# Kernel optimization log

Measured on AMD Instinct MI355X. Metric: run time of the kernel, lower is better.

The kernel has to match this reference:

```python
import jax, jax.numpy as jnp
import numpy as np

D_MODEL = 256
N_HEAD = 8
D_FF = 2048
BATCH = 4
TOK_PER_BATCH = 4096
N = BATCH * TOK_PER_BATCH  # 16384 total queries == total keys
L = 32  # neighbors per query
EPS = 1e-5


def _layer_norm(x, g, b):
    mu = jnp.mean(x, axis=-1, keepdims=True)
    var = jnp.mean(jnp.square(x - mu), axis=-1, keepdims=True)
    return (x - mu) * jax.lax.rsqrt(var + EPS) * g + b


def setup_inputs() -> dict:
    key = jax.random.key(0)
    ks = jax.random.split(key, 16)
    d, f = D_MODEL, D_FF
    s = 1.0 / np.sqrt(d)
    inp = {
        "src": jax.random.normal(ks[0], (N, d), dtype=jnp.float32),
        "index_pair": jax.random.randint(ks[1], (N, L), 0, TOK_PER_BATCH, dtype=jnp.int64),
        "query_batch_cnt": jnp.full((BATCH,), TOK_PER_BATCH, dtype=jnp.int32),
        "key_batch_cnt": jnp.full((BATCH,), TOK_PER_BATCH, dtype=jnp.int32),
        "index_pair_batch": jnp.repeat(jnp.arange(BATCH, dtype=jnp.int32), TOK_PER_BATCH),
        "Wq": jax.random.normal(ks[2], (d, d), dtype=jnp.float32) * s,
        "bq": jnp.zeros((d,), jnp.float32),
        "Wk": jax.random.normal(ks[3], (d, d), dtype=jnp.float32) * s,
        "bk": jnp.zeros((d,), jnp.float32),
        "Wv": jax.random.normal(ks[4], (d, d), dtype=jnp.float32) * s,
        "bv": jnp.zeros((d,), jnp.float32),
        "Wo": jax.random.normal(ks[5], (d, d), dtype=jnp.float32) * s,
        "bo": jnp.zeros((d,), jnp.float32),
        "W1": jax.random.normal(ks[6], (d, f), dtype=jnp.float32) * s,
        "b1": jnp.zeros((f,), jnp.float32),
        "W2": jax.random.normal(ks[7], (f, d), dtype=jnp.float32) * (1.0 / np.sqrt(f)),
        "b2": jnp.zeros((d,), jnp.float32),
        "g1": jnp.ones((d,), jnp.float32),
        "be1": jnp.zeros((d,), jnp.float32),
        "g2": jnp.ones((d,), jnp.float32),
        "be2": jnp.zeros((d,), jnp.float32),
    }
    return inp


def _attention(src, index_pair, key_batch_cnt, index_pair_batch,
               Wq, bq, Wk, bk, Wv, bv, Wo, bo):
    n, d = src.shape
    hd = d // N_HEAD
    scale = hd ** -0.5
    q = (src @ Wq + bq).reshape(n, N_HEAD, hd) * scale
    k = src @ Wk + bk
    v = src @ Wv + bv
    # exclusive cumsum -> start offset of each batch's key segment
    key_start = jnp.cumsum(key_batch_cnt) - key_batch_cnt          # [B]
    offs = key_start[index_pair_batch]                             # [N]
    valid = index_pair >= 0                                        # [N, L]
    idx = jnp.where(valid, index_pair + offs[:, None].astype(index_pair.dtype), 0)
    kg = k[idx].reshape(n, L, N_HEAD, hd)                          # gathered keys
    vg = v[idx].reshape(n, L, N_HEAD, hd)                          # gathered values
    logits = jnp.einsum("nhd,nlhd->nhl", q, kg)
    logits = jnp.where(valid[:, None, :], logits, jnp.float32(-1e9))
    attn = jax.nn.softmax(logits, axis=-1)
    out = jnp.einsum("nhl,nlhd->nhd", attn, vg).reshape(n, d)
    return out @ Wo + bo


def reference(src, index_pair, query_batch_cnt, key_batch_cnt, index_pair_batch,
              Wq, bq, Wk, bk, Wv, bv, Wo, bo, W1, b1, W2, b2, g1, be1, g2, be2):
    src2 = _attention(src, index_pair, key_batch_cnt, index_pair_batch,
                      Wq, bq, Wk, bk, Wv, bv, Wo, bo)
    x = _layer_norm(src + src2, g1, be1)
    ff = jax.nn.relu(x @ W1 + b1) @ W2 + b2
    return _layer_norm(x + ff, g2, be2)
```

## Files before the change

kernel.cpp:

```cpp
#include <hip/hip_runtime.h>
#include <hip/hip_bf16.h>
#include <cstddef>
#include <cstdint>

#define D_MODEL 256
#define N_TOK   16384
#define NHEAD   8
#define HDIM    32
#define LNEIGH  32
#define DFF     2048

#define SMEM_LN32 (8192 + 65536)

typedef short bf16x8 __attribute__((ext_vector_type(8)));
typedef float f32x4  __attribute__((ext_vector_type(4)));

__device__ __forceinline__ float b2f(short s) {
    unsigned u = ((unsigned)(unsigned short)s) << 16;
    return __builtin_bit_cast(float, u);
}

__device__ __forceinline__ void gload_lds16(const void* g, void* l) {
    auto* gp = reinterpret_cast<const __attribute__((address_space(1))) uint32_t*>(
        reinterpret_cast<uintptr_t>(g));
    auto* lp = reinterpret_cast<__attribute__((address_space(3))) uint32_t*>(
        reinterpret_cast<uintptr_t>(l));
    __builtin_amdgcn_global_load_lds(gp, lp, 16, 0, 0);
}

__global__ __launch_bounds__(256) void gemm_bt(
    const __hip_bfloat16* __restrict__ A, int lda,
    const __hip_bfloat16* __restrict__ Bt, int ldb,
    const float* __restrict__ bias,
    __hip_bfloat16* __restrict__ outb, int ldc,
    int M, int N, int K, int relu)
{
    __shared__ short Asm[2][128 * 32];
    __shared__ short Bsm[2][128 * 32];

    const int tid  = threadIdx.x;
    const int lane = tid & 63;
    const int wid  = tid >> 6;
    const int wr   = wid >> 1;
    const int wc   = wid & 1;
    const int bm   = blockIdx.y * 128;
    const int bn   = blockIdx.x * 128;

    f32x4 acc[4][4] = {};
    const int srow = lane >> 2;
    const int seg  = (lane & 3) * 8;

    auto stage = [&](int buf, int k0) {
        #pragma unroll
        for (int t = 0; t < 2; ++t) {
            int rbase = wid * 32 + t * 16;
            gload_lds16(A  + (size_t)(bm + rbase + srow) * lda + k0 + seg, &Asm[buf][rbase * 32]);
            gload_lds16(Bt + (size_t)(bn + rbase + srow) * ldb + k0 + seg, &Bsm[buf][rbase * 32]);
        }
    };

    const int nk = K >> 5;
    stage(0, 0);
    __syncthreads();

    for (int kk = 0; kk < nk; ++kk) {
        const int cur = kk & 1;
        if (kk + 1 < nk) stage(cur ^ 1, (kk + 1) << 5);

        bf16x8 a[4], b[4];
        #pragma unroll
        for (int i = 0; i < 4; ++i)
            a[i] = *(const bf16x8*)&Asm[cur][(wr * 64 + i * 16 + (lane & 15)) * 32 + (lane >> 4) * 8];
        #pragma unroll
        for (int j = 0; j < 4; ++j)
            b[j] = *(const bf16x8*)&Bsm[cur][(wc * 64 + j * 16 + (lane & 15)) * 32 + (lane >> 4) * 8];
        #pragma unroll
        for (int i = 0; i < 4; ++i)
            #pragma unroll
            for (int j = 0; j < 4; ++j)
                acc[i][j] = __builtin_amdgcn_mfma_f32_16x16x32_bf16(a[i], b[j], acc[i][j], 0, 0, 0);
        __syncthreads();
    }

    #pragma unroll
    for (int i = 0; i < 4; ++i) {
        int rbase = bm + wr * 64 + i * 16 + ((lane >> 4) << 2);
        #pragma unroll
        for (int j = 0; j < 4; ++j) {
            int col = bn + wc * 64 + j * 16 + (lane & 15);
            float bval = bias ? bias[col] : 0.0f;
            #pragma unroll
            for (int r = 0; r < 4; ++r) {
                int row = rbase + r;
                float v = acc[i][j][r] + bval;
                if (relu) v = fmaxf(v, 0.0f);
                outb[(size_t)row * ldc + col] = __float2bfloat16(v);
            }
        }
    }
}

__global__ __launch_bounds__(512) void gemm_bk64_ln32(
    const __hip_bfloat16* __restrict__ A, int lda,
    const __hip_bfloat16* __restrict__ Bt, int ldb,
    const float* __restrict__ bias,
    const float* __restrict__ residf,
    const __hip_bfloat16* __restrict__ residb,
    const float* __restrict__ g,
    const float* __restrict__ be,
    float* __restrict__ outf,
    __hip_bfloat16* __restrict__ outb,
    int K)
{
    extern __shared__ char smem[];
    short* AsmB = (short*)smem;
    short* BsmB = (short*)(smem + 8192);
    float* lnS  = (float*)smem;
    float* lnS2 = (float*)(smem + 1024);
    float* rmu  = (float*)(smem + 2048);
    float* rrs  = (float*)(smem + 2176);

    const int tid  = threadIdx.x;
    const int lane = tid & 63;
    const int wid  = tid >> 6;
    const int wr   = wid >> 2;
    const int wc   = wid & 3;
    const int bm   = blockIdx.x * 32;
    const int lo   = lane & 15;
    const int hi   = lane >> 4;

    f32x4 acc[4] = {};

    const int srow8 = lane >> 3;
    const int sc    = lane & 7;
    const int ssw   = ((sc ^ srow8) << 3);

    auto stage = [&](int buf, int k0) {
        if (wid < 4)
            gload_lds16(A + (size_t)(bm + wid * 8 + srow8) * lda + k0 + ssw,
                        AsmB + buf * 2048 + (wid * 8) * 64);
        #pragma unroll
        for (int t = 0; t < 4; ++t) {
            int rb = wid * 32 + t * 8;
            gload_lds16(Bt + (size_t)(rb + srow8) * ldb + k0 + ssw,
                        BsmB + buf * 16384 + rb * 64);
        }
    };

    const int nk = K >> 6;
    stage(0, 0);
    __syncthreads();

    for (int kk = 0; kk < nk; ++kk) {
        const int cur = kk & 1;
        if (kk + 1 < nk) stage(cur ^ 1, (kk + 1) << 6);

        const short* Ab = AsmB + cur * 2048;
        const short* Bb = BsmB + cur * 16384;
        #pragma unroll
        for (int ks = 0; ks < 2; ++ks) {
            const int csw = ((ks * 4 + hi) ^ (lo & 7)) << 3;
            bf16x8 a = *(const bf16x8*)&Ab[(wr * 16 + lo) * 64 + csw];
            bf16x8 b[4];
            #pragma unroll
            for (int j = 0; j < 4; ++j)
                b[j] = *(const bf16x8*)&Bb[(wc * 64 + j * 16 + lo) * 64 + csw];
            #pragma unroll
            for (int j = 0; j < 4; ++j)
                acc[j] = __builtin_amdgcn_mfma_f32_16x16x32_bf16(a, b[j], acc[j], 0, 0, 0);
        }
        __syncthreads();
    }

    float ps[4] = {}, ps2[4] = {};
    #pragma unroll
    for (int j = 0; j < 4; ++j) {
        int col = wc * 64 + j * 16 + lo;
        float bval = bias ? bias[col] : 0.0f;
        #pragma unroll
        for (int r = 0; r < 4; ++r) {
            int row = bm + wr * 16 + hi * 4 + r;
            float v = acc[j][r] + bval;
            size_t o = (size_t)row * 256 + col;
            if (residf) v += residf[o];
            if (residb) v += __bfloat162float(residb[o]);
            acc[j][r] = v;
            ps[r]  += v;
            ps2[r] += v * v;
        }
    }
    #pragma unroll
    for (int r = 0; r < 4; ++r) {
        #pragma unroll
        for (int m = 1; m < 16; m <<= 1) {
            ps[r]  += __shfl_xor(ps[r],  m);
            ps2[r] += __shfl_xor(ps2[r], m);
        }
    }
    if (lo == 0) {
        #pragma unroll
        for (int r = 0; r < 4; ++r) {
            int rl = wr * 16 + hi * 4 + r;
            lnS[wid * 32 + rl]  = ps[r];
            lnS2[wid * 32 + rl] = ps2[r];
        }
    }
    __syncthreads();
    if (tid < 32) {
        int base = (tid >> 4) * 4;
        float s  = lnS[base * 32 + tid] + lnS[(base + 1) * 32 + tid]
                 + lnS[(base + 2) * 32 + tid] + lnS[(base + 3) * 32 + tid];
        float s2 = lnS2[base * 32 + tid] + lnS2[(base + 1) * 32 + tid]
                 + lnS2[(base + 2) * 32 + tid] + lnS2[(base + 3) * 32 + tid];
        float mu  = s * (1.0f / 256.0f);
        float var = s2 * (1.0f / 256.0f) - mu * mu;
        rmu[tid] = mu;
        rrs[tid] = rsqrtf(var + 1e-5f);
    }
    __syncthreads();

    #pragma unroll
    for (int j = 0; j < 4; ++j) {
        int col = wc * 64 + j * 16 + lo;
        float gg = g[col], bb = be[col];
        #pragma unroll
        for (int r = 0; r < 4; ++r) {
            int rl = wr * 16 + hi * 4 + r;
            float v = (acc[j][r] - rmu[rl]) * rrs[rl] * gg + bb;
            size_t o = (size_t)(bm + rl) * 256 + col;
            if (outf) outf[o] = v;
            if (outb) outb[o] = __float2bfloat16(v);
        }
    }
}

__global__ __launch_bounds__(256) void gemm_qkv(
    const __hip_bfloat16* __restrict__ A,
    const __hip_bfloat16* __restrict__ Bt,
    const float* __restrict__ bias,
    float* __restrict__ qf,
    __hip_bfloat16* __restrict__ kvb)
{
    __shared__ short Asm[2][128 * 32];
    __shared__ short Bsm[2][128 * 32];

    const int tid  = threadIdx.x;
    const int lane = tid & 63;
    const int wid  = tid >> 6;
    const int wr   = wid >> 1;
    const int wc   = wid & 1;
    const int bm   = blockIdx.y * 128;
    const int bn   = blockIdx.x * 128;

    f32x4 acc[4][4] = {};
    const int srow = lane >> 2;
    const int seg  = (lane & 3) * 8;

    auto stage = [&](int buf, int k0) {
        #pragma unroll
        for (int t = 0; t < 2; ++t) {
            int rbase = wid * 32 + t * 16;
            gload_lds16(A  + (size_t)(bm + rbase + srow) * 256 + k0 + seg, &Asm[buf][rbase * 32]);
            gload_lds16(Bt + (size_t)(bn + rbase + srow) * 256 + k0 + seg, &Bsm[buf][rbase * 32]);
        }
    };

    stage(0, 0);
    __syncthreads();
    for (int kk = 0; kk < 8; ++kk) {
        const int cur = kk & 1;
        if (kk + 1 < 8) stage(cur ^ 1, (kk + 1) << 5);
        bf16x8 a[4], b[4];
        #pragma unroll
        for (int i = 0; i < 4; ++i)
            a[i] = *(const bf16x8*)&Asm[cur][(wr * 64 + i * 16 + (lane & 15)) * 32 + (lane >> 4) * 8];
        #pragma unroll
        for (int j = 0; j < 4; ++j)
            b[j] = *(const bf16x8*)&Bsm[cur][(wc * 64 + j * 16 + (lane & 15)) * 32 + (lane >> 4) * 8];
        #pragma unroll
        for (int i = 0; i < 4; ++i)
            #pragma unroll
            for (int j = 0; j < 4; ++j)
                acc[i][j] = __builtin_amdgcn_mfma_f32_16x16x32_bf16(a[i], b[j], acc[i][j], 0, 0, 0);
        __syncthreads();
    }

    const bool isq = (bn < 256);
    #pragma unroll
    for (int i = 0; i < 4; ++i) {
        int rbase = bm + wr * 64 + i * 16 + ((lane >> 4) << 2);
        #pragma unroll
        for (int j = 0; j < 4; ++j) {
            int col = bn + wc * 64 + j * 16 + (lane & 15);
            float bval = bias[col];
            #pragma unroll
            for (int r = 0; r < 4; ++r) {
                int row = rbase + r;
                float v = acc[i][j][r] + bval;
                if (isq) qf[(size_t)row * 256 + col] = v;
                else     kvb[(size_t)row * 512 + (col - 256)] = __float2bfloat16(v);
            }
        }
    }
}

__global__ __launch_bounds__(256) void cvt_f2b(
    const float* __restrict__ x, __hip_bfloat16* __restrict__ y, int n)
{
    int i = (blockIdx.x * 256 + threadIdx.x) * 4;
    if (i >= n) return;
    float4 v = *(const float4*)(x + i);
    y[i + 0] = __float2bfloat16(v.x);
    y[i + 1] = __float2bfloat16(v.y);
    y[i + 2] = __float2bfloat16(v.z);
    y[i + 3] = __float2bfloat16(v.w);
}

__global__ __launch_bounds__(256) void cvt_wt_tiled(
    const float* __restrict__ W, __hip_bfloat16* __restrict__ Wt,
    int K, int N, int ldo, float scale)
{
    __shared__ float t[32][33];
    const int n0 = blockIdx.x * 32;
    const int k0 = blockIdx.y * 32;
    const int tx = threadIdx.x & 31;
    const int ty = threadIdx.x >> 5;
    #pragma unroll
    for (int i = 0; i < 32; i += 8)
        t[ty + i][tx] = W[(size_t)(k0 + ty + i) * N + n0 + tx];
    __syncthreads();
    #pragma unroll
    for (int i = 0; i < 32; i += 8)
        Wt[(size_t)(n0 + ty + i) * ldo + k0 + tx] = __float2bfloat16(t[tx][ty + i] * scale);
}

__global__ __launch_bounds__(256) void cvt_w3_tiled(
    const float* __restrict__ Wa, const float* __restrict__ Wb,
    const float* __restrict__ Wc, __hip_bfloat16* __restrict__ Wt,
    float scale_a)
{
    __shared__ float t[32][33];
    const int n0 = blockIdx.x * 32;
    const int k0 = blockIdx.y * 32;
    const float* W = (n0 < 256) ? Wa : (n0 < 512 ? Wb : Wc);
    const float sc = (n0 < 256) ? scale_a : 1.0f;
    const int ncol = n0 & 255;
    const int tx = threadIdx.x & 31;
    const int ty = threadIdx.x >> 5;
    #pragma unroll
    for (int i = 0; i < 32; i += 8)
        t[ty + i][tx] = W[(size_t)(k0 + ty + i) * 256 + ncol + tx];
    __syncthreads();
    #pragma unroll
    for (int i = 0; i < 32; i += 8)
        Wt[(size_t)(n0 + ty + i) * 256 + k0 + tx] = __float2bfloat16(t[tx][ty + i] * sc);
}

__global__ __launch_bounds__(768) void make_bqkv(
    const float* __restrict__ bq, const float* __restrict__ bk,
    const float* __restrict__ bv, const int* __restrict__ kbc, int nb,
    float* __restrict__ o, int* __restrict__ ks, float qs)
{
    int i = threadIdx.x;
    if (i < 256)      o[i] = bq[i] * qs;
    else if (i < 512) o[i] = bk[i - 256];
    else              o[i] = bv[i - 512];
    if (i < nb) {
        int acc = 0;
        for (int j = 0; j < i; ++j) acc += kbc[j];
        ks[i] = acc;
    }
}

__global__ __launch_bounds__(256) void attn_wave(
    const float* __restrict__ qf,
    const __hip_bfloat16* __restrict__ kvb,
    const int* __restrict__ index_pair,
    const int* __restrict__ ipb,
    const int* __restrict__ key_start,
    __hip_bfloat16* __restrict__ out)
{
    const int w    = threadIdx.x >> 6;
    const int lane = threadIdx.x & 63;
    const int bid  = blockIdx.x;
    const int n  = (bid & 7) * 2048 + (bid >> 3) * 4 + w;
    const int c  = lane & 31;
    const int pp = lane >> 5;

    int raw = index_pair[(size_t)n * LNEIGH + c];
    int ks  = key_start[ipb[n]];
    int gi0 = (raw >= 0) ? raw + ks : -1;

    const float* qp = qf + (size_t)n * 256 + c * 8;
    float4 q0 = *(const float4*)(qp);
    float4 q1 = *(const float4*)(qp + 4);

    int gi[16];
    #pragma unroll
    for (int i = 0; i < 16; ++i) gi[i] = __shfl(gi0, 2 * i + pp);

    bf16x8 kr[16];
    #pragma unroll
    for (int i = 0; i < 16; ++i) {
        int g = gi[i] < 0 ? 0 : gi[i];
        kr[i] = *(const bf16x8*)(kvb + (size_t)g * 512 + c * 8);
    }

    float s[16];
    #pragma unroll
    for (int i = 0; i < 16; ++i) {
        float t = q0.x * b2f(kr[i][0]) + q0.y * b2f(kr[i][1])
                + q0.z * b2f(kr[i][2]) + q0.w * b2f(kr[i][3])
                + q1.x * b2f(kr[i][4]) + q1.y * b2f(kr[i][5])
                + q1.z * b2f(kr[i][6]) + q1.w * b2f(kr[i][7]);
        t += __shfl_xor(t, 1);
        t += __shfl_xor(t, 2);
        s[i] = (gi[i] < 0) ? -1e9f : t;
    }

    bf16x8 vr[16];
    #pragma unroll
    for (int i = 0; i < 16; ++i) {
        int g = gi[i] < 0 ? 0 : gi[i];
        vr[i] = *(const bf16x8*)(kvb + (size_t)g * 512 + 256 + c * 8);
    }

    float m = s[0];
    #pragma unroll
    for (int i = 1; i < 16; ++i) m = fmaxf(m, s[i]);
    m = fmaxf(m, __shfl_xor(m, 32));
    float tot = 0.0f;
    #pragma unroll
    for (int i = 0; i < 16; ++i) { s[i] = __expf(s[i] - m); tot += s[i]; }
    tot += __shfl_xor(tot, 32);
    const float inv = 1.0f / tot;

    float a[8] = {};
    #pragma unroll
    for (int i = 0; i < 16; ++i) {
        float wt = s[i] * inv;
        #pragma unroll
        for (int j = 0; j < 8; ++j) a[j] += wt * b2f(vr[i][j]);
    }
    #pragma unroll
    for (int j = 0; j < 8; ++j) a[j] += __shfl_xor(a[j], 32);

    if (pp == 0) {
        bf16x8 ov;
        #pragma unroll
        for (int j = 0; j < 8; ++j)
            ov[j] = __builtin_bit_cast(short, __float2bfloat16(a[j]));
        *(bf16x8*)((short*)out + (size_t)n * 256 + c * 8) = ov;
    }
}

extern "C" void kernel_launch(void* const* d_in, const int* in_sizes, int n_in,
                              void* d_out, int out_size, void* d_ws, size_t ws_size,
                              hipStream_t stream)
{
    const float* src = (const float*)d_in[0];
    const int*   index_pair = (const int*)d_in[1];
    const int*   kbc = (const int*)d_in[3];
    const int*   ipb = (const int*)d_in[4];
    const float* Wq = (const float*)d_in[5];
    const float* bq = (const float*)d_in[6];
    const float* Wk = (const float*)d_in[7];
    const float* bk = (const float*)d_in[8];
    const float* Wv = (const float*)d_in[9];
    const float* bv = (const float*)d_in[10];
    const float* Wo = (const float*)d_in[11];
    const float* bo = (const float*)d_in[12];
    const float* W1 = (const float*)d_in[13];
    const float* b1 = (const float*)d_in[14];
    const float* W2 = (const float*)d_in[15];
    const float* b2 = (const float*)d_in[16];
    const float* g1 = (const float*)d_in[17];
    const float* be1 = (const float*)d_in[18];
    const float* g2 = (const float*)d_in[19];
    const float* be2 = (const float*)d_in[20];
    float* out = (float*)d_out;
    const int nb = in_sizes[3];

    char* ws = (char*)d_ws;
    const size_t O_SRCBF = 0;
    const size_t O_QF    = 8388608;
    const size_t O_KVB   = 25165824;
    const size_t O_ATTN  = 41943040;
    const size_t O_HC    = 0;
    const size_t O_XBF   = 67108864;
    const size_t O_WQKV  = 75497472;
    const size_t O_WO    = O_WQKV + 768 * 256 * 2;
    const size_t O_W1    = O_WO + 256 * 256 * 2;
    const size_t O_W2    = O_W1 + (size_t)DFF * 256 * 2;
    const size_t O_BQKV  = O_W2 + (size_t)DFF * 256 * 2;
    const size_t O_KS    = O_BQKV + 768 * 4;

    __hip_bfloat16* src_bf  = (__hip_bfloat16*)(ws + O_SRCBF);
    float*          qf      = (float*)(ws + O_QF);
    __hip_bfloat16* kvb     = (__hip_bfloat16*)(ws + O_KVB);
    __hip_bfloat16* attn_bf = (__hip_bfloat16*)(ws + O_ATTN);
    __hip_bfloat16* hc      = (__hip_bfloat16*)(ws + O_HC);
    __hip_bfloat16* x_bf    = (__hip_bfloat16*)(ws + O_XBF);
    __hip_bfloat16* WqkvT   = (__hip_bfloat16*)(ws + O_WQKV);
    __hip_bfloat16* WoT     = (__hip_bfloat16*)(ws + O_WO);
    __hip_bfloat16* W1T     = (__hip_bfloat16*)(ws + O_W1);
    __hip_bfloat16* W2T     = (__hip_bfloat16*)(ws + O_W2);
    float*          bqkv    = (float*)(ws + O_BQKV);
    int*            ksbuf   = (int*)(ws + O_KS);

    const dim3 blk(256);
    const float qscale = 0.17677669529663687f;

    hipFuncSetAttribute(reinterpret_cast<const void*>(gemm_bk64_ln32),
                        hipFuncAttributeMaxDynamicSharedMemorySize, SMEM_LN32);

    cvt_f2b<<<N_TOK * D_MODEL / 4 / 256, blk, 0, stream>>>(src, src_bf, N_TOK * D_MODEL);
    cvt_w3_tiled<<<dim3(24, 8), blk, 0, stream>>>(Wq, Wk, Wv, WqkvT, qscale);
    cvt_wt_tiled<<<dim3(8, 8),  blk, 0, stream>>>(Wo, WoT, 256, 256, 256, 1.0f);
    cvt_wt_tiled<<<dim3(64, 8), blk, 0, stream>>>(W1, W1T, 256, DFF, 256, 1.0f);
    cvt_wt_tiled<<<dim3(8, 64), blk, 0, stream>>>(W2, W2T, DFF, 256, DFF, 1.0f);
    make_bqkv<<<1, 768, 0, stream>>>(bq, bk, bv, kbc, nb, bqkv, ksbuf, qscale);

    gemm_qkv<<<dim3(6, 128), blk, 0, stream>>>(src_bf, WqkvT, bqkv, qf, kvb);

    attn_wave<<<dim3(N_TOK / 4), blk, 0, stream>>>(qf, kvb, index_pair, ipb, ksbuf, attn_bf);

    gemm_bk64_ln32<<<dim3(N_TOK / 32), dim3(512), SMEM_LN32, stream>>>(
        attn_bf, 256, WoT, 256, bo, src, nullptr, g1, be1,
        nullptr, x_bf, 256);

    gemm_bt<<<dim3(16, 128), blk, 0, stream>>>(
        x_bf, 256, W1T, 256, b1, hc, DFF, N_TOK, DFF, 256, 1);

    gemm_bk64_ln32<<<dim3(N_TOK / 32), dim3(512), SMEM_LN32, stream>>>(
        hc, DFF, W2T, DFF, b2, nullptr, x_bf, g2, be2,
        out, nullptr, DFF);
}
```

Measured before the change: 152.6 us.

## Swizzle LDS layout in GEMMs and merge weight-prep kernels into one launch

The 128x128 GEMM kernels (gemm_bt and gemm_qkv) now XOR-swizzle the 8-element segment within each 32-wide LDS row, both when staging from global and when reading MFMA fragments. The aim is to cut LDS bank conflicts on the fragment reads. Separately, the four weight-transpose/convert kernels and the bias/offset kernel are merged into one 1281-block launch to remove launch overhead. The swizzle has to match exactly between the async global-to-LDS writes and the fragment reads, or results will be wrong.

```diff
diff --git a/kernel.cpp b/kernel.cpp
--- a/kernel.cpp
+++ b/kernel.cpp
@@ -48,7 +48,7 @@
 
     f32x4 acc[4][4] = {};
     const int srow = lane >> 2;
-    const int seg  = (lane & 3) * 8;
+    const int seg  = (((lane & 3) ^ (srow & 3)) << 3);
 
     auto stage = [&](int buf, int k0) {
         #pragma unroll
@@ -63,6 +63,8 @@
     stage(0, 0);
     __syncthreads();
 
+    const int csw = (((lane >> 4) ^ (lane & 3)) << 3);
+
     for (int kk = 0; kk < nk; ++kk) {
         const int cur = kk & 1;
         if (kk + 1 < nk) stage(cur ^ 1, (kk + 1) << 5);
@@ -70,10 +72,10 @@
         bf16x8 a[4], b[4];
         #pragma unroll
         for (int i = 0; i < 4; ++i)
-            a[i] = *(const bf16x8*)&Asm[cur][(wr * 64 + i * 16 + (lane & 15)) * 32 + (lane >> 4) * 8];
+            a[i] = *(const bf16x8*)&Asm[cur][(wr * 64 + i * 16 + (lane & 15)) * 32 + csw];
         #pragma unroll
         for (int j = 0; j < 4; ++j)
-            b[j] = *(const bf16x8*)&Bsm[cur][(wc * 64 + j * 16 + (lane & 15)) * 32 + (lane >> 4) * 8];
+            b[j] = *(const bf16x8*)&Bsm[cur][(wc * 64 + j * 16 + (lane & 15)) * 32 + csw];
         #pragma unroll
         for (int i = 0; i < 4; ++i)
             #pragma unroll
@@ -254,7 +256,7 @@
 
     f32x4 acc[4][4] = {};
     const int srow = lane >> 2;
-    const int seg  = (lane & 3) * 8;
+    const int seg  = (((lane & 3) ^ (srow & 3)) << 3);
 
     auto stage = [&](int buf, int k0) {
         #pragma unroll
@@ -267,16 +269,17 @@
 
     stage(0, 0);
     __syncthreads();
+    const int csw = (((lane >> 4) ^ (lane & 3)) << 3);
     for (int kk = 0; kk < 8; ++kk) {
         const int cur = kk & 1;
         if (kk + 1 < 8) stage(cur ^ 1, (kk + 1) << 5);
         bf16x8 a[4], b[4];
         #pragma unroll
         for (int i = 0; i < 4; ++i)
-            a[i] = *(const bf16x8*)&Asm[cur][(wr * 64 + i * 16 + (lane & 15)) * 32 + (lane >> 4) * 8];
+            a[i] = *(const bf16x8*)&Asm[cur][(wr * 64 + i * 16 + (lane & 15)) * 32 + csw];
         #pragma unroll
         for (int j = 0; j < 4; ++j)
-            b[j] = *(const bf16x8*)&Bsm[cur][(wc * 64 + j * 16 + (lane & 15)) * 32 + (lane >> 4) * 8];
+            b[j] = *(const bf16x8*)&Bsm[cur][(wc * 64 + j * 16 + (lane & 15)) * 32 + csw];
         #pragma unroll
         for (int i = 0; i < 4; ++i)
             #pragma unroll
@@ -316,60 +319,63 @@
     y[i + 3] = __float2bfloat16(v.w);
 }
 
-__global__ __launch_bounds__(256) void cvt_wt_tiled(
-    const float* __restrict__ W, __hip_bfloat16* __restrict__ Wt,
-    int K, int N, int ldo, float scale)
-{
+__global__ __launch_bounds__(256) void cvt_all(
+    const float* __restrict__ Wq, const float* __restrict__ Wk,
+    const float* __restrict__ Wv, const float* __restrict__ Wo,
+    const float* __restrict__ W1, const float* __restrict__ W2,
+    const float* __restrict__ bq, const float* __restrict__ bk,
+    const float* __restrict__ bv, const int* __restrict__ kbc, int nb,
+    __hip_bfloat16* __restrict__ WqkvT, __hip_bfloat16* __restrict__ WoT,
+    __hip_bfloat16* __restrict__ W1T,   __hip_bfloat16* __restrict__ W2T,
+    float* __restrict__ bqkv, int* __restrict__ ks, float qs)
+{
+    const int b = blockIdx.x;
+    if (b == 1280) {
+        int i = threadIdx.x;
+        #pragma unroll
+        for (int t = 0; t < 3; ++t, i += 256) {
+            if (i < 256)      bqkv[i] = bq[i] * qs;
+            else if (i < 512) bqkv[i] = bk[i - 256];
+            else              bqkv[i] = bv[i - 512];
+        }
+        i = threadIdx.x;
+        if (i < nb) {
+            int acc = 0;
+            for (int j = 0; j < i; ++j) acc += kbc[j];
+            ks[i] = acc;
+        }
+        return;
+    }
+
+    const float* W; __hip_bfloat16* Wt; int K, N, ldo, n0, k0; float sc = 1.0f;
+    if (b < 192) {
+        int i = b; n0 = (i % 24) * 32; k0 = (i / 24) * 32;
+        K = 256; N = 256; ldo = 256;
+        W = (n0 < 256) ? Wq : (n0 < 512 ? Wk : Wv);
+        sc = (n0 < 256) ? qs : 1.0f;
+        Wt = WqkvT;
+    } else if (b < 256) {
+        int i = b - 192; n0 = (i % 8) * 32; k0 = (i / 8) * 32;
+        K = 256; N = 256; ldo = 256; W = Wo; Wt = WoT;
+    } else if (b < 768) {
+        int i = b - 256; n0 = (i % 64) * 32; k0 = (i / 64) * 32;
+        K = 256; N = DFF; ldo = 256; W = W1; Wt = W1T;
+    } else {
+        int i = b - 768; n0 = (i % 8) * 32; k0 = (i / 8) * 32;
+        K = DFF; N = 256; ldo = DFF; W = W2; Wt = W2T;
+    }
+    const int ncol = (b < 192) ? (n0 & 255) : n0;
+
     __shared__ float t[32][33];
-    const int n0 = blockIdx.x * 32;
-    const int k0 = blockIdx.y * 32;
     const int tx = threadIdx.x & 31;
     const int ty = threadIdx.x >> 5;
     #pragma unroll
     for (int i = 0; i < 32; i += 8)
-        t[ty + i][tx] = W[(size_t)(k0 + ty + i) * N + n0 + tx];
+        t[ty + i][tx] = W[(size_t)(k0 + ty + i) * N + ncol + tx];
     __syncthreads();
     #pragma unroll
     for (int i = 0; i < 32; i += 8)
-        Wt[(size_t)(n0 + ty + i) * ldo + k0 + tx] = __float2bfloat16(t[tx][ty + i] * scale);
-}
-
-__global__ __launch_bounds__(256) void cvt_w3_tiled(
-    const float* __restrict__ Wa, const float* __restrict__ Wb,
-    const float* __restrict__ Wc, __hip_bfloat16* __restrict__ Wt,
-    float scale_a)
-{
-    __shared__ float t[32][33];
-    const int n0 = blockIdx.x * 32;
-    const int k0 = blockIdx.y * 32;
-    const float* W = (n0 < 256) ? Wa : (n0 < 512 ? Wb : Wc);
-    const float sc = (n0 < 256) ? scale_a : 1.0f;
-    const int ncol = n0 & 255;
-    const int tx = threadIdx.x & 31;
-    const int ty = threadIdx.x >> 5;
-    #pragma unroll
-    for (int i = 0; i < 32; i += 8)
-        t[ty + i][tx] = W[(size_t)(k0 + ty + i) * 256 + ncol + tx];
-    __syncthreads();
-    #pragma unroll
-    for (int i = 0; i < 32; i += 8)
-        Wt[(size_t)(n0 + ty + i) * 256 + k0 + tx] = __float2bfloat16(t[tx][ty + i] * sc);
-}
-
-__global__ __launch_bounds__(768) void make_bqkv(
-    const float* __restrict__ bq, const float* __restrict__ bk,
-    const float* __restrict__ bv, const int* __restrict__ kbc, int nb,
-    float* __restrict__ o, int* __restrict__ ks, float qs)
-{
-    int i = threadIdx.x;
-    if (i < 256)      o[i] = bq[i] * qs;
-    else if (i < 512) o[i] = bk[i - 256];
-    else              o[i] = bv[i - 512];
-    if (i < nb) {
-        int acc = 0;
-        for (int j = 0; j < i; ++j) acc += kbc[j];
-        ks[i] = acc;
-    }
+        Wt[(size_t)(n0 + ty + i) * ldo + k0 + tx] = __float2bfloat16(t[tx][ty + i] * sc);
 }
 
 __global__ __launch_bounds__(256) void attn_wave(
@@ -515,11 +521,8 @@
                         hipFuncAttributeMaxDynamicSharedMemorySize, SMEM_LN32);
 
     cvt_f2b<<<N_TOK * D_MODEL / 4 / 256, blk, 0, stream>>>(src, src_bf, N_TOK * D_MODEL);
-    cvt_w3_tiled<<<dim3(24, 8), blk, 0, stream>>>(Wq, Wk, Wv, WqkvT, qscale);
-    cvt_wt_tiled<<<dim3(8, 8),  blk, 0, stream>>>(Wo, WoT, 256, 256, 256, 1.0f);
-    cvt_wt_tiled<<<dim3(64, 8), blk, 0, stream>>>(W1, W1T, 256, DFF, 256, 1.0f);
-    cvt_wt_tiled<<<dim3(8, 64), blk, 0, stream>>>(W2, W2T, DFF, 256, DFF, 1.0f);
-    make_bqkv<<<1, 768, 0, stream>>>(bq, bk, bv, kbc, nb, bqkv, ksbuf, qscale);
+    cvt_all<<<1281, blk, 0, stream>>>(Wq, Wk, Wv, Wo, W1, W2, bq, bk, bv, kbc, nb,
+                                      WqkvT, WoT, W1T, W2T, bqkv, ksbuf, qscale);
 
     gemm_qkv<<<dim3(6, 128), blk, 0, stream>>>(src_bf, WqkvT, bqkv, qf, kvb);
 
```

Result: faster. 144.6 us (-5.3%).
